# Optimization experiments

Measured on AMD Instinct MI355X. Metric: run time of the kernel, lower is better.

The kernel has to match this reference:

```python
import jax, jax.numpy as jnp
import numpy as np

N, D = 16384, 256

def setup_inputs() -> dict:
    key = jax.random.key(0)
    k1, k2 = jax.random.split(key)
    image_features = jax.random.normal(k1, (N, D), dtype=jnp.float32)
    text_features = jax.random.normal(k2, (N, D), dtype=jnp.float32)
    logit_scale = jnp.float32(14.285714)  # exp(log(1/0.07)), typical CLIP temperature
    targets = jnp.arange(N, dtype=jnp.int64)
    return {"image_features": image_features, "text_features": text_features,
            "logit_scale": logit_scale, "targets": targets}

def _cross_entropy(logits, targets):
    # mean over rows of -log_softmax(logits)[i, targets[i]]
    logp = jax.nn.log_softmax(logits, axis=-1)
    return -jnp.mean(jnp.take_along_axis(logp, targets[:, None], axis=-1))

def reference(image_features, text_features, logit_scale, targets):
    logits = logit_scale * (image_features @ text_features.T)  # [N, N]
    image_loss = _cross_entropy(logits, targets)
    text_loss = _cross_entropy(logits.T, targets)
    return (image_loss + text_loss) / 2.0
```

## Files before the change

### kernel.cpp

```cpp
#include <hip/hip_runtime.h>

#define N_ 16384
#define D_ 256
#define LOG2E 1.4426950408889634f
#define HEXP2(x) __builtin_amdgcn_exp2f(x)

typedef __attribute__((ext_vector_type(8))) short short8;
typedef __attribute__((ext_vector_type(16))) float floatx16;

typedef __attribute__((address_space(1))) const unsigned int gu32_t;
typedef __attribute__((address_space(3))) unsigned int lu32_t;

__device__ __forceinline__ void async16(const void* g, void* l) {
  __builtin_amdgcn_global_load_lds((gu32_t*)g, (lu32_t*)l, 16, 0, 0);
}

__device__ __forceinline__ unsigned short f2bf(float x) {
  unsigned int u = __float_as_uint(x);
  u += 0x7fffu + ((u >> 16) & 1u);
  return (unsigned short)(u >> 16);
}

__device__ __forceinline__ float max3f(float a, float b, float c) {
  return fmaxf(fmaxf(a, b), c);
}

__global__ void prep_pack(const float* __restrict__ img, const float* __restrict__ txt,
                          const float* __restrict__ ls, short* __restrict__ PA,
                          short* __restrict__ PB, float* __restrict__ diag2,
                          float* __restrict__ out) {
  const int tid = threadIdx.x;
  const int t = blockIdx.x * 1024 + tid;
  const int m = tid & 31, h = (tid >> 5) & 1, ks = (tid >> 6) & 15;
  const int G = blockIdx.x;
  const int row = G * 32 + m, col = ks * 16 + h * 8;
  const float s2 = ls[0] * LOG2E;
  const float4* sa = (const float4*)(img + (size_t)row * D_ + col);
  const float4* sb = (const float4*)(txt + (size_t)row * D_ + col);
  float4 a0 = sa[0], a1 = sa[1];
  float4 b0 = sb[0], b1 = sb[1];
  short8 oa, ob;
  oa[0] = (short)f2bf(a0.x * s2); oa[1] = (short)f2bf(a0.y * s2);
  oa[2] = (short)f2bf(a0.z * s2); oa[3] = (short)f2bf(a0.w * s2);
  oa[4] = (short)f2bf(a1.x * s2); oa[5] = (short)f2bf(a1.y * s2);
  oa[6] = (short)f2bf(a1.z * s2); oa[7] = (short)f2bf(a1.w * s2);
  ob[0] = (short)f2bf(b0.x); ob[1] = (short)f2bf(b0.y);
  ob[2] = (short)f2bf(b0.z); ob[3] = (short)f2bf(b0.w);
  ob[4] = (short)f2bf(b1.x); ob[5] = (short)f2bf(b1.y);
  ob[6] = (short)f2bf(b1.z); ob[7] = (short)f2bf(b1.w);
  ((short8*)PA)[t] = oa;
  ((short8*)PB)[t] = ob;

  float d = a0.x * b0.x + a0.y * b0.y + a0.z * b0.z + a0.w * b0.w
          + a1.x * b1.x + a1.y * b1.y + a1.z * b1.z + a1.w * b1.w;
  __shared__ float red[32][33];
  red[tid >> 5][m] = d;
  __syncthreads();
  if (tid < 32) {
    float s = 0.f;
    #pragma unroll
    for (int q = 0; q < 32; ++q) s += red[q][tid];
    diag2[G * 32 + tid] = s * s2;
  }
  if (t == 0) out[0] = 0.f;
}

__global__ __launch_bounds__(256, 2)
void gemm_stats(const short* __restrict__ PA, const short* __restrict__ PB,
                float2* __restrict__ pR, float2* __restrict__ pC) {
  __shared__ __align__(16) char smem[73728];
  float* rowbuf  = (float*)(smem + 32768);
  float2* colbuf = (float2*)(smem + 71680);

  const int tid = threadIdx.x, lane = tid & 63, wv = tid >> 6;
  const int wr = wv >> 1, wc = wv & 1;
  const int m = lane & 31, h = lane >> 5;
  const int stripe = blockIdx.x, by = blockIdx.y;

  short8 areg[2][16];
  #pragma unroll
  for (int g = 0; g < 2; ++g)
    #pragma unroll
    for (int ks = 0; ks < 16; ++ks)
      areg[g][ks] = *(const short8*)(PA +
          ((size_t)((stripe * 4 + wr * 2 + g) * 16 + ks)) * 512 + lane * 8);
  asm volatile("s_waitcnt vmcnt(0)" ::: "memory");

  floatx16 acc[2][2];
  floatx16 zv;
  #pragma unroll
  for (int r = 0; r < 16; ++r) zv[r] = 0.f;

  auto issue = [&](int jj2, int c2, int bufsel) {
    const short* base = PB + ((size_t)((by * 64 + jj2 * 4) * 16) + c2 * 4 + wv) * 512 + lane * 8;
    char* dst = smem + bufsel * 16384 + wv * 1024;
    #pragma unroll
    for (int ct = 0; ct < 4; ++ct)
      async16(base + (size_t)ct * 8192, dst + ct * 4096);
  };
  auto compute = [&](int c, int bufsel, bool first) {
    char* base = smem + bufsel * 16384 + lane * 16;
    #pragma unroll
    for (int ksl = 0; ksl < 4; ++ksl) {
      short8 b0 = *(const short8*)(base + ((wc * 2 + 0) * 4 + ksl) * 1024);
      short8 b1 = *(const short8*)(base + ((wc * 2 + 1) * 4 + ksl) * 1024);
      int ks = c * 4 + ksl;
      if (first && ksl == 0) {
        acc[0][0] = __builtin_amdgcn_mfma_f32_32x32x16_bf16(areg[0][ks], b0, zv, 0, 0, 0);
        acc[1][0] = __builtin_amdgcn_mfma_f32_32x32x16_bf16(areg[1][ks], b0, zv, 0, 0, 0);
        acc[0][1] = __builtin_amdgcn_mfma_f32_32x32x16_bf16(areg[0][ks], b1, zv, 0, 0, 0);
        acc[1][1] = __builtin_amdgcn_mfma_f32_32x32x16_bf16(areg[1][ks], b1, zv, 0, 0, 0);
      } else {
        acc[0][0] = __builtin_amdgcn_mfma_f32_32x32x16_bf16(areg[0][ks], b0, acc[0][0], 0, 0, 0);
        acc[1][0] = __builtin_amdgcn_mfma_f32_32x32x16_bf16(areg[1][ks], b0, acc[1][0], 0, 0, 0);
        acc[0][1] = __builtin_amdgcn_mfma_f32_32x32x16_bf16(areg[0][ks], b1, acc[0][1], 0, 0, 0);
        acc[1][1] = __builtin_amdgcn_mfma_f32_32x32x16_bf16(areg[1][ks], b1, acc[1][1], 0, 0, 0);
      }
    }
  };

  issue(0, 0, 0);
  issue(0, 1, 1);

  float Mr = -3.0e38f, Sr = 0.f;

  for (int jj = 0; jj < 16; ++jj) {
    #pragma unroll
    for (int c = 0; c < 4; ++c) {
      if (jj == 15 && c == 3) { asm volatile("s_waitcnt vmcnt(0)" ::: "memory"); }
      else                    { asm volatile("s_waitcnt vmcnt(4)" ::: "memory"); }
      __builtin_amdgcn_s_barrier();
      asm volatile("" ::: "memory");
      compute(c, c & 1, c == 0);
      asm volatile("" ::: "memory");
      __builtin_amdgcn_s_barrier();
      asm volatile("" ::: "memory");
      int nc = c + 2;
      int jj2 = jj + (nc >> 2);
      if (jj2 < 16) issue(jj2, nc & 3, nc & 1);
    }

    float vm[4];
    #pragma unroll
    for (int q = 0; q < 4; ++q) {
      const floatx16& a = acc[q >> 1][q & 1];
      float t0 = max3f(a[0],  a[1],  a[2]);
      float t1 = max3f(a[3],  a[4],  a[5]);
      float t2 = max3f(a[6],  a[7],  a[8]);
      float t3 = max3f(a[9],  a[10], a[11]);
      float t4 = max3f(a[12], a[13], a[14]);
      vm[q] = fmaxf(max3f(t0, t1, a[15]), max3f(t2, t3, t4));
    }
    float v = fmaxf(max3f(vm[0], vm[1], vm[2]), vm[3]);
    #pragma unroll
    for (int off = 1; off < 64; off <<= 1) v = fmaxf(v, __shfl_xor(v, off));
    float msub = v - 96.f;

    #pragma unroll
    for (int rt = 0; rt < 2; ++rt)
      #pragma unroll
      for (int ctl = 0; ctl < 2; ++ctl)
        #pragma unroll
        for (int r = 0; r < 16; ++r) acc[rt][ctl][r] = HEXP2(acc[rt][ctl][r] - msub);

    #pragma unroll
    for (int ctl = 0; ctl < 2; ++ctl) {
      float cp0 = 0.f, cp1 = 0.f;
      #pragma unroll
      for (int r = 0; r < 8; ++r) {
        cp0 += acc[0][ctl][r] + acc[1][ctl][r];
        cp1 += acc[0][ctl][r + 8] + acc[1][ctl][r + 8];
      }
      float cp = cp0 + cp1;
      cp += __shfl_xor(cp, 32);
      if (h == 0) colbuf[wr * 128 + wc * 64 + ctl * 32 + m] = make_float2(msub, cp);
    }

    #pragma unroll
    for (int rt = 0; rt < 2; ++rt)
      #pragma unroll
      for (int rq = 0; rq < 4; ++rq) {
        float4 rp;
        rp.x = acc[rt][0][rq * 4 + 0] + acc[rt][1][rq * 4 + 0];
        rp.y = acc[rt][0][rq * 4 + 1] + acc[rt][1][rq * 4 + 1];
        rp.z = acc[rt][0][rq * 4 + 2] + acc[rt][1][rq * 4 + 2];
        rp.w = acc[rt][0][rq * 4 + 3] + acc[rt][1][rq * 4 + 3];
        *(float4*)&rowbuf[(wr * 64 + wc * 32 + m) * 76 + rt * 32 + rq * 8 + h * 4] = rp;
      }
    asm volatile("s_waitcnt lgkmcnt(0)" ::: "memory");
    __builtin_amdgcn_s_barrier();
    asm volatile("" ::: "memory");

    {
      float s0 = 0.f, s1 = 0.f, s2 = 0.f, s3 = 0.f;
      #pragma unroll
      for (int k = 0; k < 8; ++k) {
        s0 += rowbuf[(wr * 64 + h * 32 + k)      * 76 + wc * 32 + m];
        s1 += rowbuf[(wr * 64 + h * 32 + k + 8)  * 76 + wc * 32 + m];
        s2 += rowbuf[(wr * 64 + h * 32 + k + 16) * 76 + wc * 32 + m];
        s3 += rowbuf[(wr * 64 + h * 32 + k + 24) * 76 + wc * 32 + m];
      }
      float s = (s0 + s1) + (s2 + s3);
      s += __shfl_xor(s, 32);
      if (s > 0.f) {
        if (msub > Mr) { Sr = Sr * HEXP2(Mr - msub) + s; Mr = msub; }
        else           { Sr += s * HEXP2(msub - Mr); }
      }
    }
    if (tid < 128) {
      float2 c0 = colbuf[tid], c1 = colbuf[128 + tid];
      float M = -3.0e38f, L = 0.f;
      if (c0.y > 0.f) { M = c0.x; L = c0.y; }
      if (c1.y > 0.f) {
        if (c1.x > M) { L = L * HEXP2(M - c1.x) + c1.y; M = c1.x; }
        else          { L += c1.y * HEXP2(c1.x - M); }
      }
      pC[(size_t)stripe * N_ + by * 2048 + jj * 128 + tid] = make_float2(M, L);
    }
  }

  if (h == 0)
    pR[(size_t)by * N_ + stripe * 128 + wr * 64 + wc * 32 + m] = make_float2(Mr, Sr);
}

__global__ void merge_kernel(const float2* __restrict__ pR, const float2* __restrict__ pC,
                             const float* __restrict__ diag2, float* __restrict__ out) {
  auto mrg = [](float& M, float& L, float2 w) {
    if (w.y > 0.f) {
      if (w.x > M) { L = L * exp2f(M - w.x) + w.y; M = w.x; }
      else         { L += w.y * exp2f(w.x - M); }
    }
  };
  const int b = blockIdx.x, tid = threadIdx.x;
  float val = 0.f;

  if (b < 64) {
    int i = b * 256 + tid;
    float M = -3.0e38f, L = 0.f;
    #pragma unroll
    for (int g = 0; g < 8; ++g) mrg(M, L, pR[(size_t)g * N_ + i]);
    val = (M + log2f(fmaxf(L, 1e-45f))) - diag2[i];
  } else {
    int cb = b - 64;
    int i = cb * 32 + (tid & 31);
    int s0 = (tid >> 5) * 16;
    float M = -3.0e38f, L = 0.f;
    #pragma unroll
    for (int k = 0; k < 16; ++k) mrg(M, L, pC[(size_t)(s0 + k) * N_ + i]);
    __shared__ float2 part[8][32];
    part[tid >> 5][tid & 31] = make_float2(M, L);
    __syncthreads();
    if (tid < 32) {
      float M2 = -3.0e38f, L2 = 0.f;
      #pragma unroll
      for (int q = 0; q < 8; ++q) mrg(M2, L2, part[q][tid]);
      val = (M2 + log2f(fmaxf(L2, 1e-45f))) - diag2[cb * 32 + tid];
    }
  }

  __shared__ float red[256];
  red[tid] = val;
  __syncthreads();
  #pragma unroll
  for (int s = 128; s > 0; s >>= 1) {
    if (tid < s) red[tid] += red[tid + s];
    __syncthreads();
  }
  if (tid == 0)
    atomicAdd(out, red[0] * (0.69314718055994531f / 32768.0f));
}

extern "C" void kernel_launch(void* const* d_in, const int* in_sizes, int n_in,
                              void* d_out, int out_size, void* d_ws, size_t ws_size,
                              hipStream_t stream) {
  const float* img = (const float*)d_in[0];
  const float* txt = (const float*)d_in[1];
  const float* ls  = (const float*)d_in[2];
  float* out = (float*)d_out;

  char* ws = (char*)d_ws;
  short* PA    = (short*)(ws);
  short* PB    = (short*)(ws + 8388608);
  float* diag2 = (float*)(ws + 16777216);
  float2* pR   = (float2*)(ws + 16843008);
  float2* pC   = (float2*)(ws + 17891584);

  hipLaunchKernelGGL(prep_pack, dim3(512), dim3(1024), 0, stream, img, txt, ls, PA, PB, diag2, out);
  hipLaunchKernelGGL(gemm_stats, dim3(128, 8), dim3(256), 0, stream, PA, PB, pR, pC);
  hipLaunchKernelGGL(merge_kernel, dim3(576), dim3(256), 0, stream, pR, pC, diag2, out);
}
```

Baseline: 237.8 us.

## Quad-buffer B tiles to drop per-step barrier and shuffle-reduce row sums

The B-tile LDS staging grows from two buffers to four, so the second barrier after each MFMA compute step can be removed without a later issue overwriting a buffer still being read. The row-sum reduction now pre-reduces across lanes with xor shuffles and writes a much smaller row buffer, which each thread reads back with four float4 loads instead of 32 scalar LDS reads. This cuts barrier stalls and LDS traffic at the cost of more LDS per block, which could limit occupancy at two blocks per CU, plus extra shuffle instructions.

```diff
diff --git a/kernel.cpp b/kernel.cpp
--- a/kernel.cpp
+++ b/kernel.cpp
@@ -68,9 +68,9 @@
 __global__ __launch_bounds__(256, 2)
 void gemm_stats(const short* __restrict__ PA, const short* __restrict__ PB,
                 float2* __restrict__ pR, float2* __restrict__ pC) {
-  __shared__ __align__(16) char smem[73728];
-  float* rowbuf  = (float*)(smem + 32768);
-  float2* colbuf = (float2*)(smem + 71680);
+  __shared__ __align__(16) char smem[77824];
+  float* rowbuf2 = (float*)(smem + 65536);
+  float2* colbuf = (float2*)(smem + 75776);
 
   const int tid = threadIdx.x, lane = tid & 63, wv = tid >> 6;
   const int wr = wv >> 1, wc = wv & 1;
@@ -131,13 +131,11 @@
       else                    { asm volatile("s_waitcnt vmcnt(4)" ::: "memory"); }
       __builtin_amdgcn_s_barrier();
       asm volatile("" ::: "memory");
-      compute(c, c & 1, c == 0);
-      asm volatile("" ::: "memory");
-      __builtin_amdgcn_s_barrier();
+      compute(c, c, c == 0);
       asm volatile("" ::: "memory");
       int nc = c + 2;
       int jj2 = jj + (nc >> 2);
-      if (jj2 < 16) issue(jj2, nc & 3, nc & 1);
+      if (jj2 < 16) issue(jj2, nc & 3, nc & 3);
     }
 
     float vm[4];
@@ -176,32 +174,36 @@
       if (h == 0) colbuf[wr * 128 + wc * 64 + ctl * 32 + m] = make_float2(msub, cp);
     }
 
+    float rp[2][16];
     #pragma unroll
     for (int rt = 0; rt < 2; ++rt)
       #pragma unroll
-      for (int rq = 0; rq < 4; ++rq) {
-        float4 rp;
-        rp.x = acc[rt][0][rq * 4 + 0] + acc[rt][1][rq * 4 + 0];
-        rp.y = acc[rt][0][rq * 4 + 1] + acc[rt][1][rq * 4 + 1];
-        rp.z = acc[rt][0][rq * 4 + 2] + acc[rt][1][rq * 4 + 2];
-        rp.w = acc[rt][0][rq * 4 + 3] + acc[rt][1][rq * 4 + 3];
-        *(float4*)&rowbuf[(wr * 64 + wc * 32 + m) * 76 + rt * 32 + rq * 8 + h * 4] = rp;
-      }
+      for (int r = 0; r < 16; ++r) {
+        float x = acc[rt][0][r] + acc[rt][1][r];
+        x += __shfl_xor(x, 8);
+        x += __shfl_xor(x, 16);
+        rp[rt][r] = x;
+      }
+    #pragma unroll
+    for (int rt = 0; rt < 2; ++rt)
+      #pragma unroll
+      for (int r = 0; r < 16; ++r)
+        if ((m >> 3) == rt)
+          rowbuf2[(size_t)(wr * 64 + rt * 32 + (r & 3) + 8 * (r >> 2) + 4 * h) * 20 +
+                  wc * 8 + (m & 7)] = rp[rt][r];
+
     asm volatile("s_waitcnt lgkmcnt(0)" ::: "memory");
     __builtin_amdgcn_s_barrier();
     asm volatile("" ::: "memory");
 
     {
-      float s0 = 0.f, s1 = 0.f, s2 = 0.f, s3 = 0.f;
-      #pragma unroll
-      for (int k = 0; k < 8; ++k) {
-        s0 += rowbuf[(wr * 64 + h * 32 + k)      * 76 + wc * 32 + m];
-        s1 += rowbuf[(wr * 64 + h * 32 + k + 8)  * 76 + wc * 32 + m];
-        s2 += rowbuf[(wr * 64 + h * 32 + k + 16) * 76 + wc * 32 + m];
-        s3 += rowbuf[(wr * 64 + h * 32 + k + 24) * 76 + wc * 32 + m];
-      }
-      float s = (s0 + s1) + (s2 + s3);
-      s += __shfl_xor(s, 32);
+      const float* rb = rowbuf2 + (size_t)(wr * 64 + wc * 32 + m) * 20;
+      float4 q0 = *(const float4*)(rb + 0);
+      float4 q1 = *(const float4*)(rb + 4);
+      float4 q2 = *(const float4*)(rb + 8);
+      float4 q3 = *(const float4*)(rb + 12);
+      float s = ((q0.x + q0.y) + (q0.z + q0.w)) + ((q1.x + q1.y) + (q1.z + q1.w))
+              + ((q2.x + q2.y) + (q2.z + q2.w)) + ((q3.x + q3.y) + (q3.z + q3.w));
       if (s > 0.f) {
         if (msub > Mr) { Sr = Sr * HEXP2(Mr - msub) + s; Mr = msub; }
         else           { Sr += s * HEXP2(msub - Mr); }
```

Result: slower. 271.0 us (+14.0%).
